# Performance work log

Hardware: AMD Instinct MI355X
Metric: run time of the kernel (lower is better)

The kernel has to match this reference:

```python
import jax, jax.numpy as jnp
import numpy as np

L, H, P, R = 8192, 1024, 512, 256


def setup_inputs() -> dict:
    key = jax.random.key(0)
    ks = jax.random.split(key, 12)
    nrm = lambda k, s, std=0.01: std * jax.random.normal(k, s, dtype=jnp.float32)
    # Stable complex diagonal: |Lambda_bar| in [0.8, 0.999)
    mag = 0.8 + 0.199 * jax.random.uniform(ks[8], (P,), dtype=jnp.float32)
    phase = jnp.pi * jax.random.uniform(ks[9], (P,), dtype=jnp.float32)
    return {
        "input_sequence": jax.random.normal(ks[0], (L, H), dtype=jnp.float32),
        "F": nrm(ks[1], (R, H)),
        "H_proj": nrm(ks[2], (R, H)),
        "Delta_p": jnp.eye(R, dtype=jnp.float32),
        "Delta_r": jnp.eye(R, dtype=jnp.float32),
        "E": nrm(ks[3], (P, R)),
        "G": nrm(ks[4], (H, R)),
        "Lambda_bar_re": (mag * jnp.cos(phase)).astype(jnp.float32),
        "Lambda_bar_im": (mag * jnp.sin(phase)).astype(jnp.float32),
        "B_bar_re": nrm(ks[5], (P, H), 0.05),
        "B_bar_im": nrm(ks[6], (P, H), 0.05),
        "C_re": nrm(ks[7], (H, P), 0.05),
        "C_im": nrm(ks[10], (H, P), 0.05),
        "D": nrm(ks[11], (H, H), 0.02),
    }


def _binop(a, b):
    # Diagonal linear SSM associative combine: (lam, bu)
    return (b[0] * a[0], b[0] * a[1] + b[1])


def reference(input_sequence, F, H_proj, Delta_p, Delta_r, E, G,
              Lambda_bar_re, Lambda_bar_im, B_bar_re, B_bar_im,
              C_re, C_im, D):
    # p_k = Delta_p @ (F @ u_k), r_k = Delta_r @ (H_proj @ u_k)  -- vmapped over L via matmul
    p_seq = (input_sequence @ F.T) @ Delta_p.T            # (L, R)
    r_seq = (input_sequence @ H_proj.T) @ Delta_r.T       # (L, R)
    up_seq = jnp.concatenate([input_sequence, p_seq], axis=-1)  # (L, H+R)

    Lam = (Lambda_bar_re + 1j * Lambda_bar_im).astype(jnp.complex64)         # (P,)
    B_bar = (B_bar_re + 1j * B_bar_im).astype(jnp.complex64)                 # (P, H)
    B_ext = jnp.concatenate([B_bar, E.astype(jnp.complex64)], axis=1)        # (P, H+R)

    # Per-step driving term Bu_k = B_ext @ up_k
    Bu = up_seq.astype(jnp.complex64) @ B_ext.T                               # (L, P)
    Lam_el = jnp.broadcast_to(Lam, Bu.shape)                                  # (L, P)

    # Parallel associative scan: x_k = Lam * x_{k-1} + Bu_k
    _, xs = jax.lax.associative_scan(_binop, (Lam_el, Bu))                    # (L, P)

    C_tilde = (C_re + 1j * C_im).astype(jnp.complex64)                        # (H, P)
    # conj_sym=True branch: y_k = 2*Re(C_tilde @ x_k) + G @ r_k + D @ u_k
    y_seq = (2.0 * jnp.real(xs @ C_tilde.T)
             + r_seq @ G.T
             + input_sequence @ D.T)                                           # (L, H)
    return y_seq
```

## Files before the change

kernel.cpp:

```cpp
#include <hip/hip_runtime.h>
#include <stdint.h>

#define L_SEQ 8192
#define NCHUNK 64
#define CHUNK  128

typedef __attribute__((ext_vector_type(8))) short bf16x8;
typedef __attribute__((ext_vector_type(4))) float f32x4;

__device__ inline unsigned short f2bf(float x) {
  unsigned u = __builtin_bit_cast(unsigned, x);
  unsigned r = (u + 0x7fffu + ((u >> 16) & 1u)) >> 16;
  return (unsigned short)r;
}
__device__ inline float bf2f(unsigned short b) {
  unsigned u = ((unsigned)b) << 16;
  return __builtin_bit_cast(float, u);
}

#define GLD16(g, l)                                                            \
  __builtin_amdgcn_global_load_lds(                                            \
      (const __attribute__((address_space(1))) unsigned int*)(g),              \
      (__attribute__((address_space(3))) unsigned int*)(l), 16, 0, 0)

__global__ __launch_bounds__(256) void prep(
    const float* __restrict__ F, const float* __restrict__ Hp,
    const float* __restrict__ dP, const float* __restrict__ dR,
    const float* __restrict__ E, const float* __restrict__ G,
    const float* __restrict__ Bim, const float* __restrict__ Cre,
    const float* __restrict__ Cim, const float* __restrict__ u,
    unsigned short* __restrict__ Ft, unsigned short* __restrict__ Ht,
    unsigned short* __restrict__ dPb, unsigned short* __restrict__ dRb,
    unsigned short* __restrict__ Eb, unsigned short* __restrict__ Gb,
    unsigned short* __restrict__ W1, unsigned short* __restrict__ Wy,
    unsigned short* __restrict__ A2) {
  __shared__ float tile[32][33];
  const int b = blockIdx.x, tid = threadIdx.x;
  if (b < 512) {
    const float* src = (b < 256) ? F : Hp;
    unsigned short* dst = (b < 256) ? Ft : Ht;
    int bb = b & 255;
    int bx = bb & 31, by = bb >> 5;
    int tx = tid & 31, ty = tid >> 5;
#pragma unroll
    for (int dy = 0; dy < 32; dy += 8)
      tile[ty + dy][tx] = src[(size_t)(by * 32 + ty + dy) * 1024 + bx * 32 + tx];
    __syncthreads();
#pragma unroll
    for (int dy = 0; dy < 32; dy += 8)
      dst[(size_t)(bx * 32 + ty + dy) * 256 + by * 32 + tx] = f2bf(tile[tx][ty + dy]);
    return;
  }
  if (b < 1024) {
    const float* src;
    unsigned short* dst;
    int q;
    if (b < 576)      { src = dP; dst = dPb; q = (b - 512) * 256 + tid; }
    else if (b < 640) { src = dR; dst = dRb; q = (b - 576) * 256 + tid; }
    else if (b < 768) { src = E;  dst = Eb;  q = (b - 640) * 256 + tid; }
    else              { src = G;  dst = Gb;  q = (b - 768) * 256 + tid; }
    int e = q * 4;
    float4 v = *(const float4*)(src + e);
    ushort4 o = {f2bf(v.x), f2bf(v.y), f2bf(v.z), f2bf(v.w)};
    *(ushort4*)(dst + e) = o;
    return;
  }
  if (b < 1536) {
    int q = (b - 1024) * 256 + tid;
    int e = q * 4, p = e >> 10, j = e & 1023;
    float4 v = *(const float4*)(Bim + (size_t)p * 1024 + j);
    ushort4 o = {f2bf(v.x), f2bf(v.y), f2bf(v.z), f2bf(v.w)};
    *(ushort4*)(W1 + (size_t)(2 * p + 1) * 1024 + j) = o;
    return;
  }
  if (b < 2560) {
    int q = (b - 1536) * 256 + tid;
    int i = q >> 8, jp = (q & 255) * 2;
    float2 re = *(const float2*)(Cre + (size_t)i * 512 + jp);
    float2 im = *(const float2*)(Cim + (size_t)i * 512 + jp);
    ushort4 o = {f2bf(2.f * re.x), f2bf(-2.f * im.x), f2bf(2.f * re.y), f2bf(-2.f * im.y)};
    *(ushort4*)(Wy + (size_t)i * 2048 + 1024 + 2 * jp) = o;
    return;
  }
  {
    int q = (b - 2560) * 256 + tid;
    int e = q * 4, i = e >> 10, j = e & 1023;
    float4 v = *(const float4*)(u + (size_t)i * 1024 + j);
    ushort4 o = {f2bf(v.x), f2bf(v.y), f2bf(v.z), f2bf(v.w)};
    *(ushort4*)(A2 + (size_t)i * 2048 + j) = o;
  }
}

template <int HAS_ADD, int OUT_F32, int OUT_BF16>
__device__ __forceinline__ void gemm_body(
    const unsigned short* __restrict__ A, int lda,
    const unsigned short* __restrict__ B, int ldb,
    float* __restrict__ C, int ldc,
    unsigned short* __restrict__ Cb, int ldcb,
    const float* __restrict__ Add, int ldadd, int K, int m0, int n0,
    unsigned short* sA, unsigned short* sB) {
  const int tid = threadIdx.x;
  const int lane = tid & 63, wave = tid >> 6;
  const int wm = wave >> 1, wn = wave & 1;
  const int frow = lane & 15, fg = lane >> 4;

  const int srow = lane >> 2;
  const int scol = (lane & 3) * 8;
  const unsigned short* gA0 = A + (size_t)(m0 + wave * 32 + srow) * lda + scol;
  const unsigned short* gA1 = gA0 + (size_t)16 * lda;
  const unsigned short* gB0 = B + (size_t)(n0 + wave * 32 + srow) * ldb + scol;
  const unsigned short* gB1 = gB0 + (size_t)16 * ldb;

  f32x4 acc[4][4] = {};
  const int nt = K >> 5;

  {
    unsigned short* a0 = sA + wave * 1024;
    unsigned short* b0 = sB + wave * 1024;
    GLD16(gA0, a0); GLD16(gA1, a0 + 512);
    GLD16(gB0, b0); GLD16(gB1, b0 + 512);
  }
  __syncthreads();

  for (int t = 0; t < nt; ++t) {
    const int cur = (t & 1) * 4096;
    if (t + 1 < nt) {
      const int nxt = 4096 - cur;
      const int kt = (t + 1) * 32;
      unsigned short* a0 = sA + nxt + wave * 1024;
      unsigned short* b0 = sB + nxt + wave * 1024;
      GLD16(gA0 + kt, a0); GLD16(gA1 + kt, a0 + 512);
      GLD16(gB0 + kt, b0); GLD16(gB1 + kt, b0 + 512);
    }
    const unsigned short* bA = sA + cur;
    const unsigned short* bB = sB + cur;
    bf16x8 fa[4], fb[4];
#pragma unroll
    for (int f = 0; f < 4; ++f) {
      fa[f] = *(const bf16x8*)(bA + (wm * 64 + f * 16 + frow) * 32 + fg * 8);
      fb[f] = *(const bf16x8*)(bB + (wn * 64 + f * 16 + frow) * 32 + fg * 8);
    }
#pragma unroll
    for (int i = 0; i < 4; ++i)
#pragma unroll
      for (int j = 0; j < 4; ++j)
        acc[i][j] = __builtin_amdgcn_mfma_f32_16x16x32_bf16(fa[i], fb[j], acc[i][j], 0, 0, 0);
    __syncthreads();
  }

  const int crow4 = (lane >> 4) * 4, ccol = lane & 15;
#pragma unroll
  for (int i = 0; i < 4; ++i)
#pragma unroll
    for (int j = 0; j < 4; ++j)
#pragma unroll
      for (int q = 0; q < 4; ++q) {
        int r = m0 + wm * 64 + i * 16 + crow4 + q;
        int c = n0 + wn * 64 + j * 16 + ccol;
        float v = acc[i][j][q];
        if (HAS_ADD) v += Add[(size_t)r * ldadd + c];
        if (OUT_F32) C[(size_t)r * ldc + c] = v;
        if (OUT_BF16) Cb[(size_t)r * ldcb + c] = f2bf(v);
      }
}

template <int HAS_ADD, int OUT_F32, int OUT_BF16>
__global__ __launch_bounds__(256) void gemm_bt(
    const unsigned short* __restrict__ A, int lda,
    const unsigned short* __restrict__ B, int ldb,
    float* __restrict__ C, int ldc,
    unsigned short* __restrict__ Cb, int ldcb,
    const float* __restrict__ Add, int ldadd, int K) {
  __shared__ __align__(16) unsigned short sA[2 * 128 * 32];
  __shared__ __align__(16) unsigned short sB[2 * 128 * 32];
  gemm_body<HAS_ADD, OUT_F32, OUT_BF16>(A, lda, B, ldb, C, ldc, Cb, ldcb, Add,
                                        ldadd, K, blockIdx.x * 128,
                                        blockIdx.y * 128, sA, sB);
}

struct GemmP {
  const unsigned short* A; int lda;
  const unsigned short* B; int ldb;
  float* C; int ldc;
  unsigned short* Cb; int ldcb;
  const float* Add; int ldadd;
  int K; int gx;
};

template <int HAS_ADD, int OUT_F32, int OUT_BF16>
__global__ __launch_bounds__(256) void gemm_bt_dual(GemmP p0, GemmP p1) {
  __shared__ __align__(16) unsigned short sA[2 * 128 * 32];
  __shared__ __align__(16) unsigned short sB[2 * 128 * 32];
  GemmP p = blockIdx.z ? p1 : p0;
  if ((int)blockIdx.x >= p.gx) return;
  gemm_body<HAS_ADD, OUT_F32, OUT_BF16>(p.A, p.lda, p.B, p.ldb, p.C, p.ldc,
                                        p.Cb, p.ldcb, p.Add, p.ldadd, p.K,
                                        blockIdx.x * 128, blockIdx.y * 128, sA, sB);
}

__global__ __launch_bounds__(256) void scan_carry(const unsigned short* __restrict__ Bub,
                                                  const float* __restrict__ lre,
                                                  const float* __restrict__ lim,
                                                  float2* __restrict__ carry2) {
  int g = blockIdx.x * 256 + threadIdx.x;
  int p = g & 511, c = g >> 9;
  float ar = lre[p], ai = lim[p];
  float sr = 0.f, si = 0.f;
  const unsigned short* base = Bub + (size_t)c * CHUNK * 1024 + 2 * p;
#pragma unroll 8
  for (int i = 0; i < CHUNK; ++i) {
    unsigned w = *(const unsigned*)(base + (size_t)i * 1024);
    float br = bf2f((unsigned short)(w & 0xffff));
    float bi = bf2f((unsigned short)(w >> 16));
    float nr = ar * sr - ai * si + br;
    float ni = ar * si + ai * sr + bi;
    sr = nr; si = ni;
  }
  carry2[(size_t)p * NCHUNK + c] = make_float2(sr, si);
}

__global__ __launch_bounds__(512) void scan_prefix(const float2* __restrict__ carry2,
                                                   const float* __restrict__ lre,
                                                   const float* __restrict__ lim,
                                                   float2* __restrict__ prefix2) {
  int p = threadIdx.x;
  float ar = lre[p], ai = lim[p];
  float cr = ar, ci = ai;
#pragma unroll
  for (int s = 0; s < 7; ++s) {
    float t = cr * cr - ci * ci;
    ci = 2.f * cr * ci;
    cr = t;
  }
  float sr = 0.f, si = 0.f;
  const float2* cp = carry2 + (size_t)p * NCHUNK;
  float2* pp = prefix2 + (size_t)p * NCHUNK;
  for (int cb = 0; cb < NCHUNK; cb += 16) {
    float2 cv[16];
#pragma unroll
    for (int i = 0; i < 16; ++i) cv[i] = cp[cb + i];
#pragma unroll
    for (int i = 0; i < 16; ++i) {
      float nr = cr * sr - ci * si + cv[i].x;
      float ni = cr * si + ci * sr + cv[i].y;
      sr = nr; si = ni;
      pp[cb + i] = make_float2(sr, si);
    }
  }
}

__global__ __launch_bounds__(256) void scan_apply(const unsigned short* __restrict__ Bub,
                                                  const float* __restrict__ lre,
                                                  const float* __restrict__ lim,
                                                  const float2* __restrict__ prefix2,
                                                  unsigned short* __restrict__ A2) {
  int g = blockIdx.x * 256 + threadIdx.x;
  int p = g & 511, c = g >> 9;
  float ar = lre[p], ai = lim[p];
  float sr = 0.f, si = 0.f;
  if (c > 0) {
    float2 pr = prefix2[(size_t)p * NCHUNK + c - 1];
    sr = pr.x; si = pr.y;
  }
  const unsigned short* base = Bub + (size_t)c * CHUNK * 1024 + 2 * p;
  unsigned* ob = (unsigned*)(A2 + (size_t)c * CHUNK * 2048 + 1024 + 2 * p);
#pragma unroll 8
  for (int i = 0; i < CHUNK; ++i) {
    unsigned w = *(const unsigned*)(base + (size_t)i * 1024);
    float br = bf2f((unsigned short)(w & 0xffff));
    float bi = bf2f((unsigned short)(w >> 16));
    float nr = ar * sr - ai * si + br;
    float ni = ar * si + ai * sr + bi;
    sr = nr; si = ni;
    ob[(size_t)i * 1024] = (unsigned)f2bf(sr) | ((unsigned)f2bf(si) << 16);
  }
}

extern "C" void kernel_launch(void* const* d_in, const int* in_sizes, int n_in,
                              void* d_out, int out_size, void* d_ws, size_t ws_size,
                              hipStream_t stream) {
  const float* u   = (const float*)d_in[0];
  const float* F   = (const float*)d_in[1];
  const float* Hp  = (const float*)d_in[2];
  const float* dP  = (const float*)d_in[3];
  const float* dR  = (const float*)d_in[4];
  const float* E   = (const float*)d_in[5];
  const float* G   = (const float*)d_in[6];
  const float* lre = (const float*)d_in[7];
  const float* lim = (const float*)d_in[8];
  const float* Bre = (const float*)d_in[9];
  const float* Bim = (const float*)d_in[10];
  const float* Cre = (const float*)d_in[11];
  const float* Cim = (const float*)d_in[12];
  const float* Dm  = (const float*)d_in[13];
  float* y = (float*)d_out;

  uint8_t* ws = (uint8_t*)d_ws;
  size_t off = 0;
  auto alloc = [&](size_t bytes) {
    void* p = ws + off;
    off += (bytes + 255) & ~(size_t)255;
    return p;
  };
  unsigned short* A2  = (unsigned short*)alloc((size_t)L_SEQ * 2048 * 2);
  unsigned short* W1  = (unsigned short*)alloc((size_t)1024 * 1024 * 2);
  unsigned short* Wy  = (unsigned short*)alloc((size_t)1024 * 2048 * 2);
  unsigned short* Bub = (unsigned short*)alloc((size_t)L_SEQ * 1024 * 2);
  unsigned short* Ft  = (unsigned short*)alloc((size_t)1024 * 256 * 2);
  unsigned short* Ht  = (unsigned short*)alloc((size_t)1024 * 256 * 2);
  unsigned short* FpT = (unsigned short*)alloc((size_t)1024 * 256 * 2);
  unsigned short* HrT = (unsigned short*)alloc((size_t)1024 * 256 * 2);
  unsigned short* dPb = (unsigned short*)alloc((size_t)256 * 256 * 2);
  unsigned short* dRb = (unsigned short*)alloc((size_t)256 * 256 * 2);
  unsigned short* Eb  = (unsigned short*)alloc((size_t)512 * 256 * 2);
  unsigned short* Gb  = (unsigned short*)alloc((size_t)1024 * 256 * 2);
  float* carry  = (float*)alloc((size_t)512 * NCHUNK * 8);
  float* prefix = (float*)alloc((size_t)512 * NCHUNK * 8);
  (void)ws_size; (void)in_sizes; (void)n_in; (void)out_size;

  prep<<<10752, 256, 0, stream>>>(F, Hp, dP, dR, E, G, Bim, Cre, Cim, u,
                                  Ft, Ht, dPb, dRb, Eb, Gb, W1, Wy, A2);

  GemmP pa = {Ft, 256, dPb, 256, nullptr, 0, FpT, 256, nullptr, 0, 256, 8};
  GemmP pb = {Ht, 256, dRb, 256, nullptr, 0, HrT, 256, nullptr, 0, 256, 8};
  gemm_bt_dual<0, 0, 1><<<dim3(8, 2, 2), 256, 0, stream>>>(pa, pb);

  GemmP pc = {Eb, 256, FpT, 256, nullptr, 0, W1, 2048, Bre, 1024, 256, 4};
  GemmP pd = {Gb, 256, HrT, 256, nullptr, 0, Wy, 2048, Dm, 1024, 256, 8};
  gemm_bt_dual<1, 0, 1><<<dim3(8, 8, 2), 256, 0, stream>>>(pc, pd);

  gemm_bt<0, 0, 1><<<dim3(64, 8), 256, 0, stream>>>(A2, 2048, W1, 1024, nullptr, 0,
                                                    Bub, 1024, nullptr, 0, 1024);

  scan_carry<<<128, 256, 0, stream>>>(Bub, lre, lim, (float2*)carry);
  scan_prefix<<<1, 512, 0, stream>>>((const float2*)carry, lre, lim, (float2*)prefix);
  scan_apply<<<128, 256, 0, stream>>>(Bub, lre, lim, (const float2*)prefix, A2);

  gemm_bt<0, 1, 0><<<dim3(64, 8), 256, 0, stream>>>(A2, 2048, Wy, 2048, y, 1024,
                                                    nullptr, 0, nullptr, 0, 2048);
}
```

Measured before the change: 241.0 us.

## Halve scan chunk length, fold prefix pass into apply, swap tiny GEMM operands

```diff
diff --git a/kernel.cpp b/kernel.cpp
--- a/kernel.cpp
+++ b/kernel.cpp
@@ -2,8 +2,8 @@
 #include <stdint.h>
 
 #define L_SEQ 8192
-#define NCHUNK 64
-#define CHUNK  128
+#define NCHUNK 128
+#define CHUNK  64
 
 typedef __attribute__((ext_vector_type(8))) short bf16x8;
 typedef __attribute__((ext_vector_type(4))) float f32x4;
@@ -91,7 +91,7 @@
   }
 }
 
-template <int HAS_ADD, int OUT_F32, int OUT_BF16>
+template <int HAS_ADD, int OUT_F32, int OUT_BF16, int TRANSB16>
 __device__ __forceinline__ void gemm_body(
     const unsigned short* __restrict__ A, int lda,
     const unsigned short* __restrict__ B, int ldb,
@@ -160,7 +160,10 @@
         float v = acc[i][j][q];
         if (HAS_ADD) v += Add[(size_t)r * ldadd + c];
         if (OUT_F32) C[(size_t)r * ldc + c] = v;
-        if (OUT_BF16) Cb[(size_t)r * ldcb + c] = f2bf(v);
+        if (OUT_BF16) {
+          if (TRANSB16) Cb[(size_t)c * ldcb + r] = f2bf(v);
+          else          Cb[(size_t)r * ldcb + c] = f2bf(v);
+        }
       }
 }
 
@@ -173,9 +176,9 @@
     const float* __restrict__ Add, int ldadd, int K) {
   __shared__ __align__(16) unsigned short sA[2 * 128 * 32];
   __shared__ __align__(16) unsigned short sB[2 * 128 * 32];
-  gemm_body<HAS_ADD, OUT_F32, OUT_BF16>(A, lda, B, ldb, C, ldc, Cb, ldcb, Add,
-                                        ldadd, K, blockIdx.x * 128,
-                                        blockIdx.y * 128, sA, sB);
+  gemm_body<HAS_ADD, OUT_F32, OUT_BF16, 0>(A, lda, B, ldb, C, ldc, Cb, ldcb,
+                                           Add, ldadd, K, blockIdx.x * 128,
+                                           blockIdx.y * 128, sA, sB);
 }
 
 struct GemmP {
@@ -187,15 +190,15 @@
   int K; int gx;
 };
 
-template <int HAS_ADD, int OUT_F32, int OUT_BF16>
+template <int HAS_ADD, int OUT_F32, int OUT_BF16, int TRANSB16>
 __global__ __launch_bounds__(256) void gemm_bt_dual(GemmP p0, GemmP p1) {
   __shared__ __align__(16) unsigned short sA[2 * 128 * 32];
   __shared__ __align__(16) unsigned short sB[2 * 128 * 32];
   GemmP p = blockIdx.z ? p1 : p0;
   if ((int)blockIdx.x >= p.gx) return;
-  gemm_body<HAS_ADD, OUT_F32, OUT_BF16>(p.A, p.lda, p.B, p.ldb, p.C, p.ldc,
-                                        p.Cb, p.ldcb, p.Add, p.ldadd, p.K,
-                                        blockIdx.x * 128, blockIdx.y * 128, sA, sB);
+  gemm_body<HAS_ADD, OUT_F32, OUT_BF16, TRANSB16>(
+      p.A, p.lda, p.B, p.ldb, p.C, p.ldc, p.Cb, p.ldcb, p.Add, p.ldadd, p.K,
+      blockIdx.x * 128, blockIdx.y * 128, sA, sB);
 }
 
 __global__ __launch_bounds__(256) void scan_carry(const unsigned short* __restrict__ Bub,
@@ -216,51 +219,30 @@
     float ni = ar * si + ai * sr + bi;
     sr = nr; si = ni;
   }
-  carry2[(size_t)p * NCHUNK + c] = make_float2(sr, si);
-}
-
-__global__ __launch_bounds__(512) void scan_prefix(const float2* __restrict__ carry2,
-                                                   const float* __restrict__ lre,
-                                                   const float* __restrict__ lim,
-                                                   float2* __restrict__ prefix2) {
-  int p = threadIdx.x;
-  float ar = lre[p], ai = lim[p];
-  float cr = ar, ci = ai;
-#pragma unroll
-  for (int s = 0; s < 7; ++s) {
-    float t = cr * cr - ci * ci;
-    ci = 2.f * cr * ci;
-    cr = t;
-  }
-  float sr = 0.f, si = 0.f;
-  const float2* cp = carry2 + (size_t)p * NCHUNK;
-  float2* pp = prefix2 + (size_t)p * NCHUNK;
-  for (int cb = 0; cb < NCHUNK; cb += 16) {
-    float2 cv[16];
-#pragma unroll
-    for (int i = 0; i < 16; ++i) cv[i] = cp[cb + i];
-#pragma unroll
-    for (int i = 0; i < 16; ++i) {
-      float nr = cr * sr - ci * si + cv[i].x;
-      float ni = cr * si + ci * sr + cv[i].y;
-      sr = nr; si = ni;
-      pp[cb + i] = make_float2(sr, si);
-    }
-  }
+  carry2[(size_t)c * 512 + p] = make_float2(sr, si);
 }
 
 __global__ __launch_bounds__(256) void scan_apply(const unsigned short* __restrict__ Bub,
                                                   const float* __restrict__ lre,
                                                   const float* __restrict__ lim,
-                                                  const float2* __restrict__ prefix2,
+                                                  const float2* __restrict__ carry2,
                                                   unsigned short* __restrict__ A2) {
   int g = blockIdx.x * 256 + threadIdx.x;
   int p = g & 511, c = g >> 9;
   float ar = lre[p], ai = lim[p];
+  float cr = ar, ci = ai;
+#pragma unroll
+  for (int s = 0; s < 6; ++s) {
+    float t = cr * cr - ci * ci;
+    ci = 2.f * cr * ci;
+    cr = t;
+  }
   float sr = 0.f, si = 0.f;
-  if (c > 0) {
-    float2 pr = prefix2[(size_t)p * NCHUNK + c - 1];
-    sr = pr.x; si = pr.y;
+  for (int cc = 0; cc < c; ++cc) {
+    float2 cv = carry2[(size_t)cc * 512 + p];
+    float nr = cr * sr - ci * si + cv.x;
+    float ni = cr * si + ci * sr + cv.y;
+    sr = nr; si = ni;
   }
   const unsigned short* base = Bub + (size_t)c * CHUNK * 1024 + 2 * p;
   unsigned* ob = (unsigned*)(A2 + (size_t)c * CHUNK * 2048 + 1024 + 2 * p);
@@ -308,33 +290,31 @@
   unsigned short* Bub = (unsigned short*)alloc((size_t)L_SEQ * 1024 * 2);
   unsigned short* Ft  = (unsigned short*)alloc((size_t)1024 * 256 * 2);
   unsigned short* Ht  = (unsigned short*)alloc((size_t)1024 * 256 * 2);
-  unsigned short* FpT = (unsigned short*)alloc((size_t)1024 * 256 * 2);
-  unsigned short* HrT = (unsigned short*)alloc((size_t)1024 * 256 * 2);
+  unsigned short* S1t = (unsigned short*)alloc((size_t)1024 * 256 * 2);
+  unsigned short* S2t = (unsigned short*)alloc((size_t)1024 * 256 * 2);
   unsigned short* dPb = (unsigned short*)alloc((size_t)256 * 256 * 2);
   unsigned short* dRb = (unsigned short*)alloc((size_t)256 * 256 * 2);
   unsigned short* Eb  = (unsigned short*)alloc((size_t)512 * 256 * 2);
   unsigned short* Gb  = (unsigned short*)alloc((size_t)1024 * 256 * 2);
-  float* carry  = (float*)alloc((size_t)512 * NCHUNK * 8);
-  float* prefix = (float*)alloc((size_t)512 * NCHUNK * 8);
+  float* carry = (float*)alloc((size_t)NCHUNK * 512 * 8);
   (void)ws_size; (void)in_sizes; (void)n_in; (void)out_size;
 
   prep<<<10752, 256, 0, stream>>>(F, Hp, dP, dR, E, G, Bim, Cre, Cim, u,
                                   Ft, Ht, dPb, dRb, Eb, Gb, W1, Wy, A2);
 
-  GemmP pa = {Ft, 256, dPb, 256, nullptr, 0, FpT, 256, nullptr, 0, 256, 8};
-  GemmP pb = {Ht, 256, dRb, 256, nullptr, 0, HrT, 256, nullptr, 0, 256, 8};
-  gemm_bt_dual<0, 0, 1><<<dim3(8, 2, 2), 256, 0, stream>>>(pa, pb);
-
-  GemmP pc = {Eb, 256, FpT, 256, nullptr, 0, W1, 2048, Bre, 1024, 256, 4};
-  GemmP pd = {Gb, 256, HrT, 256, nullptr, 0, Wy, 2048, Dm, 1024, 256, 8};
-  gemm_bt_dual<1, 0, 1><<<dim3(8, 8, 2), 256, 0, stream>>>(pc, pd);
+  GemmP pa = {dPb, 256, Ft, 256, nullptr, 0, S1t, 256, nullptr, 0, 256, 2};
+  GemmP pb = {dRb, 256, Ht, 256, nullptr, 0, S2t, 256, nullptr, 0, 256, 2};
+  gemm_bt_dual<0, 0, 1, 1><<<dim3(2, 8, 2), 256, 0, stream>>>(pa, pb);
+
+  GemmP pc = {Eb, 256, S1t, 256, nullptr, 0, W1, 2048, Bre, 1024, 256, 4};
+  GemmP pd = {Gb, 256, S2t, 256, nullptr, 0, Wy, 2048, Dm, 1024, 256, 8};
+  gemm_bt_dual<1, 0, 1, 0><<<dim3(8, 8, 2), 256, 0, stream>>>(pc, pd);
 
   gemm_bt<0, 0, 1><<<dim3(64, 8), 256, 0, stream>>>(A2, 2048, W1, 1024, nullptr, 0,
                                                     Bub, 1024, nullptr, 0, 1024);
 
-  scan_carry<<<128, 256, 0, stream>>>(Bub, lre, lim, (float2*)carry);
-  scan_prefix<<<1, 512, 0, stream>>>((const float2*)carry, lre, lim, (float2*)prefix);
-  scan_apply<<<128, 256, 0, stream>>>(Bub, lre, lim, (const float2*)prefix, A2);
+  scan_carry<<<256, 256, 0, stream>>>(Bub, lre, lim, (float2*)carry);
+  scan_apply<<<256, 256, 0, stream>>>(Bub, lre, lim, (const float2*)carry, A2);
 
   gemm_bt<0, 1, 0><<<dim3(64, 8), 256, 0, stream>>>(A2, 2048, Wy, 2048, y, 1024,
                                                     nullptr, 0, nullptr, 0, 2048);
```

Measured after the change: 237.5 us. About the same (-1.4%).
